# Performance work log

Measured on AMD Instinct MI355X. Metric: run time of the kernel, lower is better.

The kernel has to match this reference:

```python
import jax, jax.numpy as jnp
import numpy as np

# module hyperparams (match init_kwargs)
C, K, S, RATIO, GC = 64, 7, 2, 2, 16
G = C // GC                      # 4 groups
KK = K * K                       # 49
NS = int(RATIO * S)              # 4
NN = NS * NS                     # 16
PAD = (K - 1) // 2               # 3
C1_IN = G * (2 * K * GC + KK)    # 1092
C1_OUT = G * NN * KK // 10       # 313
C2_OUT = G * NN * KK             # 3136
EPS = 1e-5


def _unfold(x, k, s, p):
    # torch.nn.Unfold: patches ordered (C, ki, kj) channel-major
    B, Cc, H, W = x.shape
    xp = jnp.pad(x, ((0, 0), (0, 0), (p, p), (p, p)))
    Ho = (H + 2 * p - k) // s + 1
    Wo = (W + 2 * p - k) // s + 1
    rows = jnp.arange(Ho)[:, None] * s + jnp.arange(k)[None, :]      # (Ho,k)
    cols = jnp.arange(Wo)[:, None] * s + jnp.arange(k)[None, :]      # (Wo,k)
    pat = xp[:, :, rows[:, :, None, None], cols[None, None, :, :]]   # (B,C,Ho,k,Wo,k)
    return pat.transpose(0, 1, 3, 5, 2, 4)                            # (B,C,k,k,Ho,Wo)


def setup_inputs() -> dict:
    key = jax.random.key(0)
    ks = jax.random.split(key, 5)
    x = jax.random.normal(ks[0], (8, C, 64, 64), dtype=jnp.float32)
    w1 = jax.random.normal(ks[1], (C1_OUT, C1_IN), dtype=jnp.float32) * 0.02
    gamma = jnp.ones((C1_OUT,), dtype=jnp.float32)   # BN weight (constant_init 1)
    beta = jnp.zeros((C1_OUT,), dtype=jnp.float32)   # BN bias
    w2 = jax.random.normal(ks[2], (C2_OUT, C1_OUT), dtype=jnp.float32) * 0.02
    b2 = jnp.zeros((C2_OUT,), dtype=jnp.float32)
    return {"x": x, "w1": w1, "gamma": gamma, "beta": beta, "w2": w2, "b2": b2}


def reference(x, w1, gamma, beta, w2, b2):
    B, _, H, W = x.shape
    pat = _unfold(x, K, S, PAD)                          # (B,C,K,K,Ho,Wo)
    Ho, Wo = pat.shape[-2], pat.shape[-1]
    xg = pat.reshape(B, G, GC, K, K, Ho, Wo)
    # three axis-wise max pools -> per-pixel descriptor
    x1 = xg.max(axis=2).reshape(B, G * K * K, Ho, Wo)
    x2 = xg.max(axis=3).reshape(B, G * GC * K, Ho, Wo)
    x3 = xg.max(axis=4).reshape(B, G * GC * K, Ho, Wo)
    feat = jnp.concatenate([x1, x2, x3], axis=1)         # (B, C1_IN, Ho, Wo)
    # conv1: 1x1 conv (no bias) + BN (batch stats) + ReLU
    h = jnp.einsum('bchw,oc->bohw', feat, w1)
    mu = h.mean(axis=(0, 2, 3), keepdims=True)
    var = h.var(axis=(0, 2, 3), keepdims=True)
    h = gamma[None, :, None, None] * (h - mu) * jax.lax.rsqrt(var + EPS) + beta[None, :, None, None]
    h = jax.nn.relu(h)
    # conv2: 1x1 conv with bias
    h2 = jnp.einsum('bchw,oc->bohw', h, w2) + b2[None, :, None, None]
    wt = h2.reshape(B, G, KK, NN, Ho, Wo)
    wt = jax.nn.softmax(wt, axis=2)                      # softmax over kernel positions
    # softmax-weighted patch reduction (mean over k*k)
    xk = xg.reshape(B, G, GC, KK, Ho, Wo)
    out = jnp.einsum('bgckhw,bgknhw->bgcnhw', xk, wt) / KK
    out = out.reshape(B, C, NS, NS, Ho, Wo)
    out = out.transpose(0, 1, 4, 2, 5, 3).reshape(B, C, Ho * NS, Wo * NS)
    return out
```

## Files before the change

### kernel.cpp

```cpp
#include <hip/hip_runtime.h>

namespace {
constexpr int kB    = 8;
constexpr int kC    = 64;
constexpr int kH    = 64, kW = 64;
constexpr int kNP   = 8192;
constexpr int kC1In = 1092;
constexpr int kKP   = 1152;
constexpr int kC1Out= 313;
constexpr int kC2Out= 3136;
constexpr int kC1P  = 320;
constexpr int kRowS = 56;
constexpr int kPosS = 16 * kRowS + 8;
constexpr int kPreFeat = 2048;
constexpr int kPreW2   = 490;
constexpr int kPreW1   = 1440;
constexpr int kPreBlocks = kPreFeat + kPreW2 + kPreW1;
}

typedef __attribute__((ext_vector_type(8))) short bf16x8;
typedef __attribute__((ext_vector_type(8))) _Float16 f16x8;
typedef __attribute__((ext_vector_type(2))) _Float16 h16x2;
typedef __attribute__((ext_vector_type(4))) float f32x4;

__device__ __forceinline__ unsigned short f2bf(float f) {
    unsigned u = __float_as_uint(f);
    unsigned r = (u + 0x7fffu + ((u >> 16) & 1u)) >> 16;
    return (unsigned short)r;
}

__global__ __launch_bounds__(256) void k_pre(const float* __restrict__ x,
        const float* __restrict__ w1, const float* __restrict__ w2,
        unsigned short* __restrict__ feat_bf, unsigned short* __restrict__ w1s,
        bf16x8* __restrict__ w2t, float* __restrict__ stats) {
    __shared__ float xs[16 * 7 * 40];
    int tid = threadIdx.x;
    int bid = blockIdx.x;

    if (bid < kPreFeat) {
        int g = bid >> 9, pt = bid & 511;
        int p0 = pt * 16;
        int b = p0 >> 10, i = (p0 >> 5) & 31, j0 = p0 & 31;
        int y0 = 2 * i - 3, xbase = 2 * j0 - 3;
        const float* xb = x + ((size_t)(b * 64 + g * 16) << 12);

        for (int idx = tid; idx < 16 * 7 * 40; idx += 256) {
            int ch = idx / 280, r2 = idx - ch * 280;
            int row = r2 / 40, col = r2 - row * 40;
            int yy = y0 + row, xx = xbase + col;
            float v = 0.f;
            if ((unsigned)yy < 64u && (unsigned)xx < 64u)
                v = xb[(ch << 12) + (yy << 6) + xx];
            xs[idx] = v;
        }
        __syncthreads();

        for (int o = tid; o < 16 * 273; o += 256) {
            int pos = o / 273, c = o - pos * 273;
            float m = -INFINITY;
            int cg;
            if (c < 49) {
                int a = c / 7, bk = c - a * 7;
                int base = a * 40 + 2 * pos + bk;
                #pragma unroll
                for (int ch = 0; ch < 16; ++ch) m = fmaxf(m, xs[ch * 280 + base]);
                cg = g * 49 + c;
            } else if (c < 161) {
                int r = c - 49;
                int ch = r / 7, bk = r - ch * 7;
                int base = ch * 280 + 2 * pos + bk;
                #pragma unroll
                for (int a = 0; a < 7; ++a) m = fmaxf(m, xs[base + a * 40]);
                cg = 196 + g * 112 + r;
            } else {
                int r = c - 161;
                int ch = r / 7, a = r - ch * 7;
                int base = ch * 280 + a * 40 + 2 * pos;
                #pragma unroll
                for (int bk = 0; bk < 7; ++bk) m = fmaxf(m, xs[base + bk]);
                cg = 644 + g * 112 + r;
            }
            feat_bf[(size_t)(p0 + pos) * kKP + cg] = f2bf(m);
        }
        if (g == 3) {
            for (int idx = tid; idx < 16 * 60; idx += 256) {
                int pos = idx / 60, c = idx - pos * 60;
                feat_bf[(size_t)(p0 + pos) * kKP + 1092 + c] = 0;
            }
        }
    } else if (bid < kPreFeat + kPreW2) {
        int idx = (bid - kPreFeat) * 256 + tid;
        int lane = idx & 63;
        int t = (idx >> 6) % 10;
        int k = (idx / 640) % 49;
        int g = idx / 31360;
        int n = lane & 15, c0 = t * 32 + ((lane >> 4) << 3);
        int row = g * 784 + k * 16 + n;
        bf16x8 hi;
        #pragma unroll
        for (int e = 0; e < 8; ++e) {
            int c = c0 + e;
            float v = (c < kC1Out) ? w2[(size_t)row * kC1Out + c] : 0.f;
            hi[e] = (short)f2bf(v);
        }
        w2t[idx] = hi;
    } else {
        int idx = (bid - kPreFeat - kPreW2) * 256 + tid;
        if (idx < 640) stats[idx] = 0.f;
        int r = idx / kKP, c = idx - r * kKP;
        float v = (r < kC1Out && c < kC1In) ? w1[(size_t)r * kC1In + c] : 0.f;
        w1s[idx] = f2bf(v);
    }
}

__global__ __launch_bounds__(512) void k_gemm1(
        const unsigned short* __restrict__ feat_bf, const unsigned short* __restrict__ w1s,
        float* __restrict__ h, float* __restrict__ sum_, float* __restrict__ sumsq_) {
    __shared__ unsigned short Ald[128 * 64];
    __shared__ unsigned short Bld[64 * 64];
    __shared__ float lsum[64], lsq[64];
    int tid = threadIdx.x;
    int lane = tid & 63, wv = tid >> 6;
    int row0 = blockIdx.x * 128, col0 = blockIdx.y * 64;
    int wr = wv >> 1, wc = wv & 1;
    int srow = lane >> 3;
    int soct = (lane & 7) ^ srow;
    int frow = lane & 15, fk = lane >> 4;

    f32x4 acc[2][2] = {};
    for (int k0 = 0; k0 < kKP; k0 += 64) {
        #pragma unroll
        for (int qq = 0; qq < 3; ++qq) {
            int q = wv + qq * 8;
            const unsigned short* srcbase;
            unsigned short* dst;
            int grow;
            if (q < 16) { grow = row0 + q * 8 + srow; srcbase = feat_bf; dst = Ald + q * 512; }
            else        { grow = col0 + (q - 16) * 8 + srow; srcbase = w1s; dst = Bld + (q - 16) * 512; }
            const unsigned short* src = srcbase + (size_t)grow * kKP + k0 + soct * 8;
            __builtin_amdgcn_global_load_lds(
                (const __attribute__((address_space(1))) unsigned int*)src,
                (__attribute__((address_space(3))) unsigned int*)dst, 16, 0, 0);
        }
        __syncthreads();
        #pragma unroll
        for (int ks = 0; ks < 2; ++ks) {
            int oct = ks * 4 + fk;
            bf16x8 a0, a1, b0, b1;
            { int r = wr * 32 + frow;      a0 = *(const bf16x8*)(Ald + (r * 8 + (oct ^ (r & 7))) * 8); }
            { int r = wr * 32 + 16 + frow; a1 = *(const bf16x8*)(Ald + (r * 8 + (oct ^ (r & 7))) * 8); }
            { int r = wc * 32 + frow;      b0 = *(const bf16x8*)(Bld + (r * 8 + (oct ^ (r & 7))) * 8); }
            { int r = wc * 32 + 16 + frow; b1 = *(const bf16x8*)(Bld + (r * 8 + (oct ^ (r & 7))) * 8); }
            acc[0][0] = __builtin_amdgcn_mfma_f32_16x16x32_bf16(a0, b0, acc[0][0], 0, 0, 0);
            acc[0][1] = __builtin_amdgcn_mfma_f32_16x16x32_bf16(a0, b1, acc[0][1], 0, 0, 0);
            acc[1][0] = __builtin_amdgcn_mfma_f32_16x16x32_bf16(a1, b0, acc[1][0], 0, 0, 0);
            acc[1][1] = __builtin_amdgcn_mfma_f32_16x16x32_bf16(a1, b1, acc[1][1], 0, 0, 0);
        }
        __syncthreads();
    }

    if (tid < 64) { lsum[tid] = 0.f; lsq[tid] = 0.f; }
    __syncthreads();
    #pragma unroll
    for (int i = 0; i < 2; ++i) {
        int mrow = row0 + wr * 32 + i * 16 + (lane >> 4) * 4;
        #pragma unroll
        for (int j = 0; j < 2; ++j) {
            int col_l = wc * 32 + j * 16 + (lane & 15);
            float s = 0.f, sq = 0.f;
            #pragma unroll
            for (int r = 0; r < 4; ++r) {
                float v = acc[i][j][r];
                h[(size_t)(mrow + r) * kC1P + col0 + col_l] = v;
                s += v; sq += v * v;
            }
            atomicAdd(&lsum[col_l], s);
            atomicAdd(&lsq[col_l], sq);
        }
    }
    __syncthreads();
    if (tid < 64 && col0 + tid < kC1Out) {
        atomicAdd(&sum_[col0 + tid], lsum[tid]);
        atomicAdd(&sumsq_[col0 + tid], lsq[tid]);
    }
}

__global__ void k_split_h(const float* __restrict__ h,
                          const float* __restrict__ sum_, const float* __restrict__ sumsq_,
                          const float* __restrict__ gamma, const float* __restrict__ beta,
                          bf16x8* __restrict__ ht_hi) {
    int idx = blockIdx.x * 256 + threadIdx.x;
    int lane = idx & 63;
    int t = (idx >> 6) % 10;
    int ptile = idx / 640;
    int pos = ptile * 16 + (lane & 15);
    int c0 = t * 32 + ((lane >> 4) << 3);
    float vv[8];
    *(float4*)&vv[0] = *(const float4*)(h + (size_t)pos * kC1P + c0);
    *(float4*)&vv[4] = *(const float4*)(h + (size_t)pos * kC1P + c0 + 4);
    bf16x8 hi;
    #pragma unroll
    for (int e = 0; e < 8; ++e) {
        int c = c0 + e;
        float v = 0.f;
        if (c < kC1Out) {
            float mu  = sum_[c]   * (1.f / kNP);
            float var = sumsq_[c] * (1.f / kNP) - mu * mu;
            float sc  = gamma[c] * rsqrtf(var + 1e-5f);
            float sh  = beta[c] - mu * sc;
            v = fmaxf(vv[e] * sc + sh, 0.f);
        }
        hi[e] = (short)f2bf(v);
    }
    ht_hi[idx] = hi;
}

__global__ __launch_bounds__(512) void k_fused(
        const bf16x8* __restrict__ ht_hi, const bf16x8* __restrict__ w2t,
        const float* __restrict__ b2, const float* __restrict__ x,
        float* __restrict__ out) {
    __shared__ _Float16 wtb[32 * kPosS];
    __shared__ float invt[512];
    __shared__ bf16x8 htl[1280];
    int tid = threadIdx.x;
    int lane = tid & 63, wv = tid >> 6;
    int bid = blockIdx.x;
    int g = bid >> 8, pt = bid & 255;

    {
        const bf16x8* hb = ht_hi + (size_t)(pt * 2) * 640;
        #pragma unroll
        for (int r = 0; r < 3; ++r) {
            int idx = r * 512 + tid;
            if (idx < 1280)
                __builtin_amdgcn_global_load_lds(
                    (const __attribute__((address_space(1))) unsigned int*)(hb + idx),
                    (__attribute__((address_space(3))) unsigned int*)(htl + idx), 16, 0, 0);
        }
    }
    __syncthreads();

    int col = lane & 15, rgrp = lane >> 4;
    for (int k = wv; k < 49; k += 8) {
        f32x4 acc0 = {0.f, 0.f, 0.f, 0.f};
        f32x4 acc1 = {0.f, 0.f, 0.f, 0.f};
        const bf16x8* wb = w2t + ((size_t)(g * 49 + k) * 10) * 64 + lane;
        #pragma unroll
        for (int t = 0; t < 10; ++t) {
            bf16x8 bh = wb[t * 64];
            bf16x8 a0 = htl[t * 64 + lane];
            bf16x8 a1 = htl[640 + t * 64 + lane];
            acc0 = __builtin_amdgcn_mfma_f32_16x16x32_bf16(a0, bh, acc0, 0, 0, 0);
            acc1 = __builtin_amdgcn_mfma_f32_16x16x32_bf16(a1, bh, acc1, 0, 0, 0);
        }
        float bias = b2[g * 784 + k * 16 + col];
        #pragma unroll
        for (int r = 0; r < 4; ++r) {
            int pos = rgrp * 4 + r;
            wtb[pos * kPosS + k * 16 + col]        = (_Float16)(acc0[r] + bias);
            wtb[(pos + 16) * kPosS + k * 16 + col] = (_Float16)(acc1[r] + bias);
        }
    }
    __syncthreads();

    {
        int pos = tid >> 4, n = tid & 15;
        const _Float16* baseA = wtb + pos * kPosS + n;
        f16x8 ee[7];
        float m = -INFINITY;
        #pragma unroll
        for (int c = 0; c < 7; ++c)
            #pragma unroll
            for (int e = 0; e < 8; ++e) {
                int k = c * 8 + e;
                if (k < 49) {
                    _Float16 v = baseA[k * 16];
                    ee[c][e] = v;
                    m = fmaxf(m, (float)v);
                } else ee[c][e] = (_Float16)0.f;
            }
        float s = 0.f;
        #pragma unroll
        for (int c = 0; c < 7; ++c)
            #pragma unroll
            for (int e = 0; e < 8; ++e) {
                int k = c * 8 + e;
                if (k < 49) {
                    float ex = __expf((float)ee[c][e] - m);
                    s += ex;
                    ee[c][e] = (_Float16)ex;
                }
            }
        __syncthreads();
        _Float16* baseB = wtb + pos * kPosS + n * kRowS;
        #pragma unroll
        for (int c = 0; c < 7; ++c) *(f16x8*)(baseB + c * 8) = ee[c];
        invt[tid] = 1.f / (s * 49.f);
    }
    __syncthreads();

    {
        int pos = tid & 31, c16 = tid >> 5;
        int p = pt * 32 + pos;
        int b = p >> 10, i = (p >> 5) & 31, j = p & 31;
        int y0 = 2 * i - 3, x0c = 2 * j - 3;
        const float* xc = x + (((size_t)b * 64 + g * 16 + c16) << 12);
        h16x2 patch2[28];
        #pragma unroll
        for (int a = 0; a < 7; ++a) {
            int yy = y0 + a;
            #pragma unroll
            for (int bk = 0; bk < 7; ++bk) {
                int kk = a * 7 + bk, xx = x0c + bk;
                float v = ((unsigned)yy < 64u && (unsigned)xx < 64u)
                        ? xc[(yy << 6) + xx] : 0.f;
                patch2[kk >> 1][kk & 1] = (_Float16)v;
            }
        }
        patch2[24][1] = (_Float16)0.f;
        patch2[25] = (h16x2)(_Float16)0.f;
        patch2[26] = (h16x2)(_Float16)0.f;
        patch2[27] = (h16x2)(_Float16)0.f;

        const _Float16* prow = wtb + pos * kPosS;
        float* outb = out + (((size_t)b * 64 + g * 16 + c16) << 14);
        #pragma unroll
        for (int n1 = 0; n1 < 4; ++n1) {
            f32x4 st;
            #pragma unroll
            for (int n2 = 0; n2 < 4; ++n2) {
                int n = n1 * 4 + n2;
                const f16x8* row = (const f16x8*)(prow + n * kRowS);
                float acc = 0.f;
                #pragma unroll
                for (int c = 0; c < 7; ++c) {
                    f16x8 w = row[c];
                    #pragma unroll
                    for (int q = 0; q < 4; ++q) {
                        h16x2 wp; wp[0] = w[2 * q]; wp[1] = w[2 * q + 1];
                        acc = __builtin_amdgcn_fdot2(patch2[c * 4 + q], wp, acc, false);
                    }
                }
                st[n2] = acc * invt[pos * 16 + n];
            }
            *(f32x4*)(outb + (i * 4 + n1) * 128 + j * 4) = st;
        }
    }
}

extern "C" void kernel_launch(void* const* d_in, const int* in_sizes, int n_in,
                              void* d_out, int out_size, void* d_ws, size_t ws_size,
                              hipStream_t stream) {
    const float* x     = (const float*)d_in[0];
    const float* w1    = (const float*)d_in[1];
    const float* gamma = (const float*)d_in[2];
    const float* beta  = (const float*)d_in[3];
    const float* w2    = (const float*)d_in[4];
    const float* b2    = (const float*)d_in[5];
    float* out = (float*)d_out;

    float* ws = (float*)d_ws;
    unsigned short* feat_bf = (unsigned short*)ws;
    float* h       = ws + 4718592;
    float* w2t_f   = h + 2621440;
    unsigned short* w1s = (unsigned short*)(w2t_f + 501760);
    float* sum_   = w2t_f + 501760 + 184320;
    float* sumsq_ = sum_ + 320;

    bf16x8* ht_hi = (bf16x8*)ws;
    bf16x8* w2t   = (bf16x8*)w2t_f;

    k_pre<<<kPreBlocks, 256, 0, stream>>>(x, w1, w2, feat_bf, w1s, w2t, sum_);
    k_gemm1<<<dim3(kNP / 128, 5), 512, 0, stream>>>(feat_bf, w1s, h, sum_, sumsq_);
    k_split_h<<<1280, 256, 0, stream>>>(h, sum_, sumsq_, gamma, beta, ht_hi);
    k_fused<<<1024, 512, 0, stream>>>(ht_hi, w2t, b2, x, out);
}
```

Measured before the change: 118.9 us.

## Fuse BN-ReLU bf16 conversion into fused kernel and prefetch w2 tiles

Removes the separate k_split_h launch: the fused kernel now loads raw fp32 h rows into shared memory, applies batch-norm and ReLU, and converts to bf16 in shared memory before the second GEMM. It also double-buffers the w2 fragment loads in registers so the next kernel-position's weights are fetched while the current MFMAs run. This saves one launch and the bf16 intermediate round trip. In exchange, each of the four group blocks sharing a pixel tile now redoes the normalization, and register pressure rises.

```diff
diff --git a/kernel.cpp b/kernel.cpp
--- a/kernel.cpp
+++ b/kernel.cpp
@@ -185,40 +185,12 @@
     }
 }
 
-__global__ void k_split_h(const float* __restrict__ h,
-                          const float* __restrict__ sum_, const float* __restrict__ sumsq_,
-                          const float* __restrict__ gamma, const float* __restrict__ beta,
-                          bf16x8* __restrict__ ht_hi) {
-    int idx = blockIdx.x * 256 + threadIdx.x;
-    int lane = idx & 63;
-    int t = (idx >> 6) % 10;
-    int ptile = idx / 640;
-    int pos = ptile * 16 + (lane & 15);
-    int c0 = t * 32 + ((lane >> 4) << 3);
-    float vv[8];
-    *(float4*)&vv[0] = *(const float4*)(h + (size_t)pos * kC1P + c0);
-    *(float4*)&vv[4] = *(const float4*)(h + (size_t)pos * kC1P + c0 + 4);
-    bf16x8 hi;
-    #pragma unroll
-    for (int e = 0; e < 8; ++e) {
-        int c = c0 + e;
-        float v = 0.f;
-        if (c < kC1Out) {
-            float mu  = sum_[c]   * (1.f / kNP);
-            float var = sumsq_[c] * (1.f / kNP) - mu * mu;
-            float sc  = gamma[c] * rsqrtf(var + 1e-5f);
-            float sh  = beta[c] - mu * sc;
-            v = fmaxf(vv[e] * sc + sh, 0.f);
-        }
-        hi[e] = (short)f2bf(v);
-    }
-    ht_hi[idx] = hi;
-}
-
 __global__ __launch_bounds__(512) void k_fused(
-        const bf16x8* __restrict__ ht_hi, const bf16x8* __restrict__ w2t,
-        const float* __restrict__ b2, const float* __restrict__ x,
-        float* __restrict__ out) {
+        const float* __restrict__ h,
+        const float* __restrict__ sum_, const float* __restrict__ sumsq_,
+        const float* __restrict__ gamma, const float* __restrict__ beta,
+        const bf16x8* __restrict__ w2t, const float* __restrict__ b2,
+        const float* __restrict__ x, float* __restrict__ out) {
     __shared__ _Float16 wtb[32 * kPosS];
     __shared__ float invt[512];
     __shared__ bf16x8 htl[1280];
@@ -227,38 +199,83 @@
     int bid = blockIdx.x;
     int g = bid >> 8, pt = bid & 255;
 
+    float* hst = (float*)wtb;
     {
-        const bf16x8* hb = ht_hi + (size_t)(pt * 2) * 640;
-        #pragma unroll
-        for (int r = 0; r < 3; ++r) {
+        const float* hb = h + (size_t)pt * 32 * kC1P;
+        #pragma unroll
+        for (int r = 0; r < 5; ++r) {
             int idx = r * 512 + tid;
-            if (idx < 1280)
-                __builtin_amdgcn_global_load_lds(
-                    (const __attribute__((address_space(1))) unsigned int*)(hb + idx),
-                    (__attribute__((address_space(3))) unsigned int*)(htl + idx), 16, 0, 0);
-        }
+            __builtin_amdgcn_global_load_lds(
+                (const __attribute__((address_space(1))) unsigned int*)(hb + idx * 4),
+                (__attribute__((address_space(3))) unsigned int*)(hst + idx * 4), 16, 0, 0);
+        }
+    }
+    __syncthreads();
+
+    for (int v = tid; v < 1280; v += 512) {
+        int lv = v & 63;
+        int t = (v >> 6) % 10;
+        int half = v / 640;
+        int pos = half * 16 + (lv & 15);
+        int c0 = t * 32 + ((lv >> 4) << 3);
+        float vv[8];
+        *(float4*)&vv[0] = *(const float4*)(hst + pos * kC1P + c0);
+        *(float4*)&vv[4] = *(const float4*)(hst + pos * kC1P + c0 + 4);
+        bf16x8 hi;
+        #pragma unroll
+        for (int e = 0; e < 8; ++e) {
+            int c = c0 + e;
+            float vo = 0.f;
+            if (c < kC1Out) {
+                float mu  = sum_[c]   * (1.f / kNP);
+                float var = sumsq_[c] * (1.f / kNP) - mu * mu;
+                float sc  = gamma[c] * rsqrtf(var + 1e-5f);
+                float sh  = beta[c] - mu * sc;
+                vo = fmaxf(vv[e] * sc + sh, 0.f);
+            }
+            hi[e] = (short)f2bf(vo);
+        }
+        htl[v] = hi;
     }
     __syncthreads();
 
     int col = lane & 15, rgrp = lane >> 4;
-    for (int k = wv; k < 49; k += 8) {
-        f32x4 acc0 = {0.f, 0.f, 0.f, 0.f};
-        f32x4 acc1 = {0.f, 0.f, 0.f, 0.f};
-        const bf16x8* wb = w2t + ((size_t)(g * 49 + k) * 10) * 64 + lane;
-        #pragma unroll
-        for (int t = 0; t < 10; ++t) {
-            bf16x8 bh = wb[t * 64];
-            bf16x8 a0 = htl[t * 64 + lane];
-            bf16x8 a1 = htl[640 + t * 64 + lane];
-            acc0 = __builtin_amdgcn_mfma_f32_16x16x32_bf16(a0, bh, acc0, 0, 0, 0);
-            acc1 = __builtin_amdgcn_mfma_f32_16x16x32_bf16(a1, bh, acc1, 0, 0, 0);
-        }
-        float bias = b2[g * 784 + k * 16 + col];
-        #pragma unroll
-        for (int r = 0; r < 4; ++r) {
-            int pos = rgrp * 4 + r;
-            wtb[pos * kPosS + k * 16 + col]        = (_Float16)(acc0[r] + bias);
-            wtb[(pos + 16) * kPosS + k * 16 + col] = (_Float16)(acc1[r] + bias);
+    const bf16x8* wbase = w2t + (size_t)g * 49 * 640 + lane;
+    {
+        bf16x8 cur[10], nxt[10];
+        int k = wv;
+        {
+            const bf16x8* wb = wbase + (size_t)k * 640;
+            #pragma unroll
+            for (int t = 0; t < 10; ++t) cur[t] = wb[t * 64];
+        }
+        while (k < 49) {
+            int kn = k + 8;
+            if (kn < 49) {
+                const bf16x8* wb = wbase + (size_t)kn * 640;
+                #pragma unroll
+                for (int t = 0; t < 10; ++t) nxt[t] = wb[t * 64];
+            }
+            __builtin_amdgcn_sched_barrier(0);
+            f32x4 acc0 = {0.f,0.f,0.f,0.f};
+            f32x4 acc1 = {0.f,0.f,0.f,0.f};
+            #pragma unroll
+            for (int t = 0; t < 10; ++t) {
+                bf16x8 a0 = htl[t * 64 + lane];
+                bf16x8 a1 = htl[640 + t * 64 + lane];
+                acc0 = __builtin_amdgcn_mfma_f32_16x16x32_bf16(a0, cur[t], acc0, 0, 0, 0);
+                acc1 = __builtin_amdgcn_mfma_f32_16x16x32_bf16(a1, cur[t], acc1, 0, 0, 0);
+            }
+            float bias = b2[g * 784 + k * 16 + col];
+            #pragma unroll
+            for (int r = 0; r < 4; ++r) {
+                int pos = rgrp * 4 + r;
+                wtb[pos * kPosS + k * 16 + col]        = (_Float16)(acc0[r] + bias);
+                wtb[(pos + 16) * kPosS + k * 16 + col] = (_Float16)(acc1[r] + bias);
+            }
+            #pragma unroll
+            for (int t = 0; t < 10; ++t) cur[t] = nxt[t];
+            k = kn;
         }
     }
     __syncthreads();
@@ -367,11 +384,9 @@
     float* sum_   = w2t_f + 501760 + 184320;
     float* sumsq_ = sum_ + 320;
 
-    bf16x8* ht_hi = (bf16x8*)ws;
-    bf16x8* w2t   = (bf16x8*)w2t_f;
+    bf16x8* w2t = (bf16x8*)w2t_f;
 
     k_pre<<<kPreBlocks, 256, 0, stream>>>(x, w1, w2, feat_bf, w1s, w2t, sum_);
     k_gemm1<<<dim3(kNP / 128, 5), 512, 0, stream>>>(feat_bf, w1s, h, sum_, sumsq_);
-    k_split_h<<<1280, 256, 0, stream>>>(h, sum_, sumsq_, gamma, beta, ht_hi);
-    k_fused<<<1024, 512, 0, stream>>>(ht_hi, w2t, b2, x, out);
-}
+    k_fused<<<1024, 512, 0, stream>>>(h, sum_, sumsq_, gamma, beta, w2t, b2, x, out);
+}
```

Result: slower. 124.6 us (+4.8%).

## Switch conv2 GEMM to 32x32x16 MFMA with repacked weight and activation layouts

Applied to the files above, without the earlier changes.

Replaces the pair of 16x16x32 bf16 MFMAs per kernel position with a single 32x32x16 MFMA. Each wave now covers 32 positions by 32 output columns (two kernel positions), iterating 25 column tiles instead of 49. The w2 and h operands are repacked into matching 32-wide layouts, which pads w2 to 800 rows per group and grows the workspace. It also raises wave priority around the MFMA loop. This cuts global weight loads and instruction count per output, at the cost of an idle padded tile at k=49 and a different scatter pattern into the LDS softmax buffer.

```diff
diff --git a/kernel.cpp b/kernel.cpp
--- a/kernel.cpp
+++ b/kernel.cpp
@@ -13,7 +13,7 @@
 constexpr int kRowS = 56;
 constexpr int kPosS = 16 * kRowS + 8;
 constexpr int kPreFeat = 2048;
-constexpr int kPreW2   = 490;
+constexpr int kPreW2   = 500;
 constexpr int kPreW1   = 1440;
 constexpr int kPreBlocks = kPreFeat + kPreW2 + kPreW1;
 }
@@ -22,6 +22,7 @@
 typedef __attribute__((ext_vector_type(8))) _Float16 f16x8;
 typedef __attribute__((ext_vector_type(2))) _Float16 h16x2;
 typedef __attribute__((ext_vector_type(4))) float f32x4;
+typedef __attribute__((ext_vector_type(16))) float f32x16;
 
 __device__ __forceinline__ unsigned short f2bf(float f) {
     unsigned u = __float_as_uint(f);
@@ -32,7 +33,7 @@
 __global__ __launch_bounds__(256) void k_pre(const float* __restrict__ x,
         const float* __restrict__ w1, const float* __restrict__ w2,
         unsigned short* __restrict__ feat_bf, unsigned short* __restrict__ w1s,
-        bf16x8* __restrict__ w2t, float* __restrict__ stats) {
+        bf16x8* __restrict__ w2t32, float* __restrict__ stats) {
     __shared__ float xs[16 * 7 * 40];
     int tid = threadIdx.x;
     int bid = blockIdx.x;
@@ -91,19 +92,23 @@
     } else if (bid < kPreFeat + kPreW2) {
         int idx = (bid - kPreFeat) * 256 + tid;
         int lane = idx & 63;
-        int t = (idx >> 6) % 10;
-        int k = (idx / 640) % 49;
-        int g = idx / 31360;
-        int n = lane & 15, c0 = t * 32 + ((lane >> 4) << 3);
-        int row = g * 784 + k * 16 + n;
-        bf16x8 hi;
-        #pragma unroll
-        for (int e = 0; e < 8; ++e) {
-            int c = c0 + e;
-            float v = (c < kC1Out) ? w2[(size_t)row * kC1Out + c] : 0.f;
-            hi[e] = (short)f2bf(v);
-        }
-        w2t[idx] = hi;
+        int t = (idx >> 6) % 20;
+        int p = (idx / 1280) % 25;
+        int g = idx / 32000;
+        int nu = lane & 31, o = lane >> 5;
+        int cv = p * 32 + nu;
+        int c0 = t * 16 + o * 8;
+        bf16x8 hi = {};
+        if (cv < 784) {
+            int row = g * 784 + cv;
+            #pragma unroll
+            for (int e = 0; e < 8; ++e) {
+                int c = c0 + e;
+                float v = (c < kC1Out) ? w2[(size_t)row * kC1Out + c] : 0.f;
+                hi[e] = (short)f2bf(v);
+            }
+        }
+        w2t32[idx] = hi;
     } else {
         int idx = (bid - kPreFeat - kPreW2) * 256 + tid;
         if (idx < 640) stats[idx] = 0.f;
@@ -188,16 +193,15 @@
 __global__ void k_split_h(const float* __restrict__ h,
                           const float* __restrict__ sum_, const float* __restrict__ sumsq_,
                           const float* __restrict__ gamma, const float* __restrict__ beta,
-                          bf16x8* __restrict__ ht_hi) {
+                          bf16x8* __restrict__ ht32) {
     int idx = blockIdx.x * 256 + threadIdx.x;
-    int lane = idx & 63;
-    int t = (idx >> 6) % 10;
-    int ptile = idx / 640;
-    int pos = ptile * 16 + (lane & 15);
-    int c0 = t * 32 + ((lane >> 4) << 3);
+    int pt = idx / 1280, r = idx - pt * 1280;
+    int t2o = r >> 5, pos = r & 31;
+    int c0 = (t2o >> 1) * 16 + (t2o & 1) * 8;
+    int gpos = pt * 32 + pos;
     float vv[8];
-    *(float4*)&vv[0] = *(const float4*)(h + (size_t)pos * kC1P + c0);
-    *(float4*)&vv[4] = *(const float4*)(h + (size_t)pos * kC1P + c0 + 4);
+    *(float4*)&vv[0] = *(const float4*)(h + (size_t)gpos * kC1P + c0);
+    *(float4*)&vv[4] = *(const float4*)(h + (size_t)gpos * kC1P + c0 + 4);
     bf16x8 hi;
     #pragma unroll
     for (int e = 0; e < 8; ++e) {
@@ -212,11 +216,11 @@
         }
         hi[e] = (short)f2bf(v);
     }
-    ht_hi[idx] = hi;
+    ht32[idx] = hi;
 }
 
 __global__ __launch_bounds__(512) void k_fused(
-        const bf16x8* __restrict__ ht_hi, const bf16x8* __restrict__ w2t,
+        const bf16x8* __restrict__ ht32, const bf16x8* __restrict__ w2t32,
         const float* __restrict__ b2, const float* __restrict__ x,
         float* __restrict__ out) {
     __shared__ _Float16 wtb[32 * kPosS];
@@ -228,7 +232,7 @@
     int g = bid >> 8, pt = bid & 255;
 
     {
-        const bf16x8* hb = ht_hi + (size_t)(pt * 2) * 640;
+        const bf16x8* hb = ht32 + (size_t)pt * 1280;
         #pragma unroll
         for (int r = 0; r < 3; ++r) {
             int idx = r * 512 + tid;
@@ -240,25 +244,27 @@
     }
     __syncthreads();
 
-    int col = lane & 15, rgrp = lane >> 4;
-    for (int k = wv; k < 49; k += 8) {
-        f32x4 acc0 = {0.f, 0.f, 0.f, 0.f};
-        f32x4 acc1 = {0.f, 0.f, 0.f, 0.f};
-        const bf16x8* wb = w2t + ((size_t)(g * 49 + k) * 10) * 64 + lane;
-        #pragma unroll
-        for (int t = 0; t < 10; ++t) {
-            bf16x8 bh = wb[t * 64];
-            bf16x8 a0 = htl[t * 64 + lane];
-            bf16x8 a1 = htl[640 + t * 64 + lane];
-            acc0 = __builtin_amdgcn_mfma_f32_16x16x32_bf16(a0, bh, acc0, 0, 0, 0);
-            acc1 = __builtin_amdgcn_mfma_f32_16x16x32_bf16(a1, bh, acc1, 0, 0, 0);
-        }
-        float bias = b2[g * 784 + k * 16 + col];
-        #pragma unroll
-        for (int r = 0; r < 4; ++r) {
-            int pos = rgrp * 4 + r;
-            wtb[pos * kPosS + k * 16 + col]        = (_Float16)(acc0[r] + bias);
-            wtb[(pos + 16) * kPosS + k * 16 + col] = (_Float16)(acc1[r] + bias);
+    int nu = lane & 31, h5 = lane >> 5;
+    int aidx = h5 * 32 + nu;
+    for (int p = wv; p < 25; p += 8) {
+        const bf16x8* wb = w2t32 + ((size_t)(g * 25 + p) * 20) * 64 + lane;
+        f32x16 acc = {};
+        __builtin_amdgcn_s_setprio(1);
+        #pragma unroll
+        for (int t = 0; t < 20; ++t) {
+            bf16x8 b = wb[t * 64];
+            bf16x8 a = htl[t * 64 + aidx];
+            acc = __builtin_amdgcn_mfma_f32_32x32x16_bf16(a, b, acc, 0, 0, 0);
+        }
+        __builtin_amdgcn_s_setprio(0);
+        int k = 2 * p + (nu >> 4), n = nu & 15;
+        if (k < 49) {
+            float bias = b2[g * 784 + k * 16 + n];
+            #pragma unroll
+            for (int r = 0; r < 16; ++r) {
+                int pos = (r & 3) + 8 * (r >> 2) + 4 * h5;
+                wtb[pos * kPosS + k * 16 + n] = (_Float16)(acc[r] + bias);
+            }
         }
     }
     __syncthreads();
@@ -363,15 +369,15 @@
     unsigned short* feat_bf = (unsigned short*)ws;
     float* h       = ws + 4718592;
     float* w2t_f   = h + 2621440;
-    unsigned short* w1s = (unsigned short*)(w2t_f + 501760);
-    float* sum_   = w2t_f + 501760 + 184320;
+    unsigned short* w1s = (unsigned short*)(w2t_f + 512000);
+    float* sum_   = w2t_f + 512000 + 184320;
     float* sumsq_ = sum_ + 320;
 
-    bf16x8* ht_hi = (bf16x8*)ws;
-    bf16x8* w2t   = (bf16x8*)w2t_f;
-
-    k_pre<<<kPreBlocks, 256, 0, stream>>>(x, w1, w2, feat_bf, w1s, w2t, sum_);
+    bf16x8* ht32  = (bf16x8*)ws;
+    bf16x8* w2t32 = (bf16x8*)w2t_f;
+
+    k_pre<<<kPreBlocks, 256, 0, stream>>>(x, w1, w2, feat_bf, w1s, w2t32, sum_);
     k_gemm1<<<dim3(kNP / 128, 5), 512, 0, stream>>>(feat_bf, w1s, h, sum_, sumsq_);
-    k_split_h<<<1280, 256, 0, stream>>>(h, sum_, sumsq_, gamma, beta, ht_hi);
-    k_fused<<<1024, 512, 0, stream>>>(ht_hi, w2t, b2, x, out);
-}
+    k_split_h<<<1280, 256, 0, stream>>>(h, sum_, sumsq_, gamma, beta, ht32);
+    k_fused<<<1024, 512, 0, stream>>>(ht32, w2t32, b2, x, out);
+}
```

After: 123.5 us. 1.04x slower.
